# Kernel tuning notes

Hardware: AMD Instinct MI355X
Metric: run time of the kernel (lower is better)

## Reference

```python
import jax, jax.numpy as jnp
import numpy as np

# Config derived from init_kwargs
DIM = 256
DSTATE = 64
DCONV = 3
HEADDIM = 64
CHUNK = 256
NGROUPS = 1
DINNER = int(2.0 * DIM)                 # 512
NHEADS = DINNER // HEADDIM              # 8
CONVDIM = DINNER + 2 * NGROUPS * DSTATE  # 640 (x, B, C share the depthwise conv)
DPROJ = 2 * DINNER + 2 * NGROUPS * DSTATE + NHEADS  # z + xBC + dt


def setup_inputs() -> dict:
    key = jax.random.key(0)
    ks = jax.random.split(key, 8)
    B, H, W = 8, 64, 64
    return dict(
        x=jax.random.normal(ks[0], (B, DIM, H, W), jnp.float32),
        ln_w=jnp.ones((DIM,), jnp.float32),
        ln_b=jnp.zeros((DIM,), jnp.float32),
        in_proj_w=jax.random.normal(ks[1], (DPROJ, DIM), jnp.float32) * 0.02,
        conv_w=jax.random.normal(ks[2], (CONVDIM, 1, DCONV, DCONV), jnp.float32) * 0.1,
        conv_b=jnp.zeros((CONVDIM,), jnp.float32),
        A_log=jnp.log(jax.random.uniform(ks[3], (NHEADS,), jnp.float32, 1.0, 16.0)),
        D=jnp.ones((NHEADS,), jnp.float32),
        dt_bias=jax.random.uniform(ks[4], (NHEADS,), jnp.float32, -2.0, 0.0),
        rms_w=jnp.ones((DINNER,), jnp.float32),
        out_proj_w=jax.random.normal(ks[5], (DIM, DINNER), jnp.float32) * 0.02,
    )


def _ssd(X, dA, Bm, Cm, chunk):
    """Mamba2 SSD chunked parallel scan.
    X:  (b, l, h, p)  inputs already multiplied by dt
    dA: (b, l, h)     dt * A (negative)
    Bm, Cm: (b, l, h, n)
    """
    b, l, h, p = X.shape
    n = Bm.shape[-1]
    c = l // chunk
    q = chunk
    Xc = X.reshape(b, c, q, h, p)
    Bc = Bm.reshape(b, c, q, h, n)
    Cc = Cm.reshape(b, c, q, h, n)
    Ac = dA.reshape(b, c, q, h).transpose(0, 3, 1, 2)            # (b,h,c,q)
    Acs = jnp.cumsum(Ac, axis=-1)                                # (b,h,c,q)
    # intra-chunk (diagonal blocks): causal decay matrix L
    tri = jnp.tril(jnp.ones((q, q), bool))
    Ldec = jnp.where(tri, jnp.exp(Acs[..., :, None] - Acs[..., None, :]), 0.0)
    Y_diag = jnp.einsum('bcqhn,bcshn,bhcqs,bcshp->bcqhp', Cc, Bc, Ldec, Xc)
    # per-chunk final states
    decay_states = jnp.exp(Acs[..., -1:] - Acs)                  # (b,h,c,q)
    states = jnp.einsum('bcqhn,bhcq,bcqhp->bchpn', Bc, decay_states, Xc)
    # inter-chunk recurrence (segment-sum over chunk totals)
    A_last = jnp.pad(Acs[..., -1], ((0, 0), (0, 0), (1, 0)))     # (b,h,c+1)
    ccs = jnp.cumsum(A_last, axis=-1)
    tric = jnp.tril(jnp.ones((c + 1, c + 1), bool))
    decay_chunk = jnp.where(tric, jnp.exp(ccs[..., :, None] - ccs[..., None, :]), 0.0)
    states0 = jnp.concatenate([jnp.zeros_like(states[:, :1]), states], axis=1)
    prev = jnp.einsum('bhzc,bchpn->bzhpn', decay_chunk, states0)[:, :-1]
    # contribution of carried-in state (off-diagonal blocks)
    Y_off = jnp.einsum('bcqhn,bchpn,bhcq->bcqhp', Cc, prev, jnp.exp(Acs))
    return (Y_diag + Y_off).reshape(b, l, h, p)


def _forward(x, ln_w, ln_b, in_proj_w, conv_w, conv_b, A_log, D, dt_bias, rms_w, out_proj_w):
    Bn, Cd, Hh, Ww = x.shape
    L = Hh * Ww
    # LayerNorm over channel dim (channel-first LayerNorm2d)
    mu = jnp.mean(x, axis=1, keepdims=True)
    var = jnp.mean((x - mu) ** 2, axis=1, keepdims=True)
    xn = (x - mu) * jax.lax.rsqrt(var + 1e-5)
    xn = xn * ln_w[None, :, None, None] + ln_b[None, :, None, None]
    # input projection (1x1): -> z | xBC | dt
    zxbcdt = jnp.einsum('bchw,dc->bdhw', xn, in_proj_w)
    z = zxbcdt[:, :DINNER]
    xBC = zxbcdt[:, DINNER:DINNER + CONVDIM]
    dt = zxbcdt[:, DINNER + CONVDIM:]                            # (b, nheads, H, W)
    # depthwise 2D conv + SiLU on xBC
    xBC = jax.lax.conv_general_dilated(
        xBC, conv_w, (1, 1), 'SAME',
        dimension_numbers=('NCHW', 'OIHW', 'NCHW'), feature_group_count=CONVDIM)
    xBC = jax.nn.silu(xBC + conv_b[None, :, None, None])
    # flatten spatial -> sequence, channel-last
    def to_seq(t):
        return t.reshape(Bn, t.shape[1], L).transpose(0, 2, 1)
    xBC, dt, z = to_seq(xBC), to_seq(dt), to_seq(z)
    xs = xBC[..., :DINNER].reshape(Bn, L, NHEADS, HEADDIM)
    Bg = xBC[..., DINNER:DINNER + NGROUPS * DSTATE].reshape(Bn, L, NGROUPS, DSTATE)
    Cg = xBC[..., DINNER + NGROUPS * DSTATE:].reshape(Bn, L, NGROUPS, DSTATE)
    hpg = NHEADS // NGROUPS
    Bm = jnp.repeat(Bg, hpg, axis=2)
    Cm = jnp.repeat(Cg, hpg, axis=2)
    dt = jax.nn.softplus(dt + dt_bias[None, None, :])            # (b, L, nheads)
    A = -jnp.exp(A_log)
    y = _ssd(xs * dt[..., None], dt * A[None, None, :], Bm, Cm, CHUNK)
    y = y + D[None, None, :, None] * xs                          # skip connection
    y = y.reshape(Bn, L, DINNER)
    # gated RMSNorm: norm(y * silu(z)) * w
    y = y * jax.nn.silu(z)
    y = y * jax.lax.rsqrt(jnp.mean(y * y, axis=-1, keepdims=True) + 1e-5) * rms_w
    out = jnp.einsum('bld,cd->blc', y, out_proj_w)
    out = out.transpose(0, 2, 1).reshape(Bn, Cd, Hh, Ww)
    return x + out                                               # residual


def reference(x, ln_w, ln_b, in_proj_w, conv_w, conv_b, A_log, D, dt_bias, rms_w, out_proj_w):
    return _forward(x, ln_w, ln_b, in_proj_w, conv_w, conv_b, A_log, D, dt_bias, rms_w, out_proj_w)
```

## Files before the change

### kernel.cpp

```cpp
#include <hip/hip_runtime.h>
#include <hip/hip_bf16.h>
#include <math.h>

#define DIMC   256
#define LSP    4096
#define BATCH  8
#define DINNER 512
#define NHEADS 8
#define HEADDIM 64
#define DSTATE 64
#define CONVDIM 640
#define DPROJ  1160
#define MPAD   1280
#define CHUNK  256
#define NCHUNK 16

typedef unsigned short u16;
typedef __attribute__((ext_vector_type(8))) unsigned short u16x8;
typedef __attribute__((ext_vector_type(8))) short s16x8;
typedef __attribute__((ext_vector_type(4))) float f32x4;

#define MFMA16(a,b,c) __builtin_amdgcn_mfma_f32_16x16x32_bf16((s16x8)(a),(s16x8)(b),(c),0,0,0)

__device__ __forceinline__ float bf2f(u16 u){ return __uint_as_float(((unsigned int)u)<<16); }
__device__ __forceinline__ u16 f2bf(float f){
  unsigned int x = __float_as_uint(f);
  unsigned int r = (x + 0x7fffu + ((x>>16)&1u)) >> 16;
  return (u16)r;
}
__device__ __forceinline__ float softplusf(float x){ return (x > 20.f) ? x : __logf(1.f + __expf(x)); }
__device__ __forceinline__ float siluf(float x){ return x * __builtin_amdgcn_rcpf(1.f + __expf(-x)); }

__global__ void convert_w(const float* __restrict__ src, u16* __restrict__ dst,
                          int total, int valid){
  int i = blockIdx.x*256 + threadIdx.x;
  if (i >= total) return;
  dst[i] = (i < valid) ? f2bf(src[i]) : (u16)0;
}

__global__ void convert_w_rms(const float* __restrict__ src, const float* __restrict__ rmsw,
                              u16* __restrict__ dst){
  int i = blockIdx.x*256 + threadIdx.x;
  if (i >= DIMC*DINNER) return;
  dst[i] = f2bf(src[i] * rmsw[i & (DINNER-1)]);
}

__global__ void ln_kernel(const float* __restrict__ X, const float* __restrict__ lnw,
                          const float* __restrict__ lnb, u16* __restrict__ XNT) {
  int pos = blockIdx.x*256 + threadIdx.x;
  int b = pos >> 12, l = pos & (LSP-1);
  const float* xb = X + ((size_t)b*DIMC)*LSP + l;
  float sum=0.f, sq=0.f;
  for (int c=0;c<DIMC;c++){ float v=xb[(size_t)c*LSP]; sum+=v; sq+=v*v; }
  float mu = sum*(1.f/DIMC);
  float var = sq*(1.f/DIMC) - mu*mu;
  float rs = rsqrtf(var + 1e-5f);
  u16* ob = XNT + ((size_t)(b*LSP + l))*DIMC;
  for (int c0=0;c0<DIMC;c0+=8){
    u16x8 v8;
    #pragma unroll
    for(int j=0;j<8;j++){
      float v = xb[(size_t)(c0+j)*LSP];
      v8[j] = f2bf((v-mu)*rs*lnw[c0+j] + lnb[c0+j]);
    }
    *(u16x8*)&ob[c0] = v8;
  }
}

__global__ __launch_bounds__(256,2) void gemm_in_fused(
    const u16* __restrict__ W, const u16* __restrict__ XNT,
    u16* __restrict__ ZT, u16* __restrict__ XBC, u16* __restrict__ DT){
  __shared__ u16 Xs[128][264];
  __shared__ u16 Ws[128][32];
  int tid=threadIdx.x, w=tid>>6, lane=tid&63, l15=lane&15, quad=lane>>4;
  int n0=blockIdx.x*128, mh=blockIdx.y, b=blockIdx.z;
  {
    const u16* src = XNT + ((size_t)(b*LSP + n0))*DIMC;
    #pragma unroll
    for (int i=0;i<16;i++){
      int g = i*256 + tid;
      int row = g>>5, c8 = (g&31)*8;
      *(u16x8*)&Xs[row][c8] = *(const u16x8*)&src[(size_t)row*DIMC + c8];
    }
  }
  for (int pti=0; pti<5; pti++){
    int ptg = mh*5 + pti;
    int m0 = ptg*128;
    f32x4 acc[4][4];
    #pragma unroll
    for(int i=0;i<4;i++)
      #pragma unroll
      for(int j=0;j<4;j++) acc[i][j]=(f32x4){0.f,0.f,0.f,0.f};
    for (int k0=0;k0<DIMC;k0+=32){
      __syncthreads();
      {
        int ch = tid*2;
        int r = ch>>2, o=(ch&3)*8;
        *(u16x8*)&Ws[r][o] = *(const u16x8*)&W[(size_t)(m0+r)*DIMC + k0 + o];
        ch++; r = ch>>2; o=(ch&3)*8;
        *(u16x8*)&Ws[r][o] = *(const u16x8*)&W[(size_t)(m0+r)*DIMC + k0 + o];
      }
      __syncthreads();
      u16x8 af[4], bfr[4];
      if (ptg < 4){
        #pragma unroll
        for(int mt=0;mt<4;mt++) af[mt] = *(const u16x8*)&Xs[(w>>1)*64+mt*16+l15][k0+quad*8];
        #pragma unroll
        for(int nt=0;nt<4;nt++) bfr[nt] = *(const u16x8*)&Ws[(w&1)*64+nt*16+l15][quad*8];
      } else {
        #pragma unroll
        for(int mt=0;mt<4;mt++) af[mt] = *(const u16x8*)&Ws[(w>>1)*64+mt*16+l15][quad*8];
        #pragma unroll
        for(int nt=0;nt<4;nt++) bfr[nt] = *(const u16x8*)&Xs[(w&1)*64+nt*16+l15][k0+quad*8];
      }
      #pragma unroll
      for(int mt=0;mt<4;mt++)
        #pragma unroll
        for(int nt=0;nt<4;nt++)
          acc[mt][nt]=MFMA16(af[mt],bfr[nt],acc[mt][nt]);
    }
    if (ptg < 4){
      #pragma unroll
      for(int mt=0;mt<4;mt++)
        #pragma unroll
        for(int nt=0;nt<4;nt++)
          #pragma unroll
          for(int r=0;r<4;r++){
            int lrow = n0 + (w>>1)*64 + mt*16 + quad*4 + r;
            int dcol = m0 + (w&1)*64 + nt*16 + l15;
            ZT[((size_t)b*LSP + lrow)*DINNER + dcol] = f2bf(acc[mt][nt][r]);
          }
    } else {
      #pragma unroll
      for(int mt=0;mt<4;mt++)
        #pragma unroll
        for(int nt=0;nt<4;nt++)
          #pragma unroll
          for(int r=0;r<4;r++){
            int prow = m0 + (w>>1)*64 + mt*16 + quad*4 + r;
            if (prow>=DPROJ) continue;
            int col = n0 + (w&1)*64 + nt*16 + l15;
            u16 v = f2bf(acc[mt][nt][r]);
            if (prow<DINNER+CONVDIM)  XBC[((size_t)b*CONVDIM+(prow-DINNER))*LSP+col]=v;
            else                      DT[((size_t)b*NHEADS+(prow-DINNER-CONVDIM))*LSP+col]=v;
          }
    }
  }
}

__global__ void gemm_out_mfma(const u16* __restrict__ A, const u16* __restrict__ Bm,
                              const float* __restrict__ Res, float* __restrict__ Out){
  __shared__ u16 As[128][32];
  __shared__ u16 Bs[128][32];
  __shared__ float rinv[128];
  int tid=threadIdx.x, w=tid>>6, lane=tid&63, l15=lane&15, quad=lane>>4;
  int b=blockIdx.z, m0=blockIdx.y*128, n0=blockIdx.x*128;
  const u16* Bb = Bm + ((size_t)b*LSP + n0)*DINNER;
  f32x4 acc[4][4];
  #pragma unroll
  for(int i=0;i<4;i++)
    #pragma unroll
    for(int j=0;j<4;j++) acc[i][j] = (f32x4){0.f,0.f,0.f,0.f};
  float sqacc = 0.f;
  for (int k0=0;k0<DINNER;k0+=32){
    __syncthreads();
    {
      int ch = tid*2;
      int r = ch>>2, o=(ch&3)*8;
      *(u16x8*)&As[r][o] = *(const u16x8*)&A[(size_t)(m0+r)*DINNER + k0 + o];
      u16x8 bv = *(const u16x8*)&Bb[(size_t)r*DINNER + k0 + o];
      *(u16x8*)&Bs[r][o] = bv;
      #pragma unroll
      for(int j=0;j<8;j++){ float f=bf2f(bv[j]); sqacc += f*f; }
      ch++; r = ch>>2; o=(ch&3)*8;
      *(u16x8*)&As[r][o] = *(const u16x8*)&A[(size_t)(m0+r)*DINNER + k0 + o];
      u16x8 bv2 = *(const u16x8*)&Bb[(size_t)r*DINNER + k0 + o];
      *(u16x8*)&Bs[r][o] = bv2;
      #pragma unroll
      for(int j=0;j<8;j++){ float f=bf2f(bv2[j]); sqacc += f*f; }
    }
    __syncthreads();
    u16x8 af[4], bfr[4];
    #pragma unroll
    for(int mt=0;mt<4;mt++) af[mt] = *(const u16x8*)&As[(w>>1)*64+mt*16+l15][quad*8];
    #pragma unroll
    for(int nt=0;nt<4;nt++) bfr[nt] = *(const u16x8*)&Bs[(w&1)*64+nt*16+l15][quad*8];
    #pragma unroll
    for(int mt=0;mt<4;mt++)
      #pragma unroll
      for(int nt=0;nt<4;nt++)
        acc[mt][nt]=MFMA16(af[mt],bfr[nt],acc[mt][nt]);
  }
  {
    float tot = sqacc + __shfl_xor(sqacc, 1, 64);
    if ((tid&1)==0) rinv[tid>>1] = rsqrtf(tot*(1.f/DINNER) + 1e-5f);
  }
  __syncthreads();
  #pragma unroll
  for(int mt=0;mt<4;mt++)
    #pragma unroll
    for(int nt=0;nt<4;nt++){
      float rv = rinv[(w&1)*64 + nt*16 + l15];
      #pragma unroll
      for(int r=0;r<4;r++){
        int row = m0 + (w>>1)*64 + mt*16 + quad*4 + r;
        int col = n0 + (w&1)*64 + nt*16 + l15;
        size_t oi = ((size_t)b*DIMC+row)*LSP+col;
        Out[oi] = acc[mt][nt][r]*rv + Res[oi];
      }
    }
}

__global__ void conv_kernel(u16* __restrict__ XBC, const float* __restrict__ CW,
                            const float* __restrict__ CB){
  int ch = blockIdx.x, b = blockIdx.y, tid = threadIdx.x;
  __shared__ float plane[66*66];
  u16* base = XBC + ((size_t)b*CONVDIM + ch)*LSP;
  for (int idx=tid; idx<66*66; idx+=256){
    int yy = idx/66 - 1, xx = idx%66 - 1;
    float v = 0.f;
    if (yy>=0 && yy<64 && xx>=0 && xx<64) v = bf2f(base[yy*64+xx]);
    plane[idx] = v;
  }
  float wg[9];
  #pragma unroll
  for (int t=0;t<9;t++) wg[t] = CW[ch*9+t];
  float bias = CB[ch];
  __syncthreads();
  for (int r=0;r<16;r++){
    int pix = tid + r*256;
    int y = pix>>6, x = pix&63;
    float s=0.f;
    #pragma unroll
    for(int dy=0;dy<3;dy++)
      #pragma unroll
      for(int dx=0;dx<3;dx++) s += plane[(y+dy)*66 + x+dx]*wg[dy*3+dx];
    base[pix] = f2bf(siluf(s + bias));
  }
}

__global__ void ssd_pre_kernel(const u16* __restrict__ DT, const float* __restrict__ A_log,
                               const float* __restrict__ dt_bias, float* __restrict__ ACS,
                               float* __restrict__ DTV, float* __restrict__ DASUM){
  int c=blockIdx.x, h=blockIdx.y, b=blockIdx.z, tid=threadIdx.x;
  __shared__ float acs[CHUNK];
  size_t base = ((size_t)b*NHEADS+h)*LSP + c*CHUNK + tid;
  float raw = bf2f(DT[base]);
  float dtv = softplusf(raw + dt_bias[h]);
  float Ah = -__expf(A_log[h]);
  acs[tid] = dtv*Ah;
  __syncthreads();
  for(int o=1;o<256;o<<=1){
    float add=(tid>=o)?acs[tid-o]:0.f;
    __syncthreads(); acs[tid]+=add; __syncthreads();
  }
  ACS[base] = acs[tid];
  DTV[base] = dtv;
  if (tid==CHUNK-1) DASUM[((size_t)b*NHEADS+h)*NCHUNK+c] = acs[tid];
}

__global__ __launch_bounds__(256,4) void ssd_states_mfma(
    const float* __restrict__ ACS, const float* __restrict__ DTV,
    const float* __restrict__ DASUM, const u16* __restrict__ XBC,
    float* __restrict__ STATES){
  int c=blockIdx.x, h=blockIdx.y, b=blockIdx.z;
  int tid=threadIdx.x, w=tid>>6, lane=tid&63, l15=lane&15, quad=lane>>4;
  __shared__ float wdt[CHUNK];
  __shared__ u16 Xw[64][136];
  __shared__ u16 Bn[64][136];
  {
    size_t base = ((size_t)b*NHEADS+h)*LSP + c*CHUNK + tid;
    float atot = DASUM[((size_t)b*NHEADS+h)*NCHUNK+c];
    wdt[tid] = DTV[base]*__expf(atot - ACS[base]);
  }
  __syncthreads();
  f32x4 acc[4];
  #pragma unroll
  for(int i=0;i<4;i++) acc[i] = (f32x4){0.f,0.f,0.f,0.f};
  size_t cb = (size_t)c*CHUNK;
  for(int th=0; th<2; th++){
    __syncthreads();
    {
      int n=tid&63, q4=tid>>6;
      const u16* Xg = XBC + ((size_t)b*CONVDIM + h*HEADDIM + n)*LSP + cb + th*128;
      const u16* Bg = XBC + ((size_t)b*CONVDIM + DINNER + n)*LSP + cb + th*128;
      #pragma unroll
      for(int i=0;i<4;i++){
        int o = q4*32+i*8;
        u16x8 v = *(const u16x8*)&Xg[o];
        u16x8 wv;
        #pragma unroll
        for(int j=0;j<8;j++) wv[j]=f2bf(bf2f(v[j])*wdt[th*128+o+j]);
        *(u16x8*)&Xw[n][o]=wv;
        *(u16x8*)&Bn[n][o] = *(const u16x8*)&Bg[o];
      }
    }
    __syncthreads();
    #pragma unroll
    for(int k8=0;k8<4;k8++){
      u16x8 a = *(const u16x8*)&Xw[w*16+l15][k8*32+quad*8];
      #pragma unroll
      for(int nt=0;nt<4;nt++){
        u16x8 bb = *(const u16x8*)&Bn[nt*16+l15][k8*32+quad*8];
        acc[nt]=MFMA16(a,bb,acc[nt]);
      }
    }
  }
  float* dst = STATES + (((size_t)b*NHEADS+h)*NCHUNK+c)*4096;
  #pragma unroll
  for(int nt=0;nt<4;nt++)
    #pragma unroll
    for(int r=0;r<4;r++)
      dst[(w*16+quad*4+r)*64 + nt*16+l15] = acc[nt][r];
}

__global__ void ssd_scan_kernel(const float* __restrict__ STATES, const float* __restrict__ DASUM,
                                u16* __restrict__ PREVB){
  int g = blockIdx.x, h = blockIdx.y, b = blockIdx.z, tid = threadIdx.x;
  int e = g*256 + tid;
  size_t hb = (size_t)b*NHEADS + h;
  size_t base = hb*NCHUNK*4096 + e;
  float s = 0.f;
  for (int cc=0;cc<NCHUNK;cc++){
    PREVB[base + (size_t)cc*4096] = f2bf(s);
    s = s*__expf(DASUM[hb*NCHUNK + cc]) + STATES[base + (size_t)cc*4096];
  }
}

__global__ __launch_bounds__(256,3) void ssd_y_mfma(
    const float* __restrict__ ACS, const float* __restrict__ DTV,
    const u16* __restrict__ XBC, const float* __restrict__ Dp,
    const u16* __restrict__ PREVB, const u16* __restrict__ ZT,
    u16* __restrict__ YG){
  int hp = blockIdx.x, bx = blockIdx.y, b = blockIdx.z;
  int h0 = hp*2;
  int c = bx>>2, tb = 3-(bx&3);
  int tid=threadIdx.x, w=tid>>6, lane=tid&63, l15=lane&15, quad=lane>>4;
  __shared__ float acs2[2][CHUNK];
  __shared__ float dtv2[2][CHUNK];
  __shared__ u16 Bs[64][72];
  __shared__ u16 Xs[2][64][72];
  __shared__ u16 Ps[2][64][72];
  {
    size_t base0 = ((size_t)b*NHEADS+h0)*LSP + c*CHUNK + tid;
    acs2[0][tid] = ACS[base0];
    dtv2[0][tid] = DTV[base0];
    acs2[1][tid] = ACS[base0 + LSP];
    dtv2[1][tid] = DTV[base0 + LSP];
  }
  u16x8 ca0, ca1;
  {
    const u16* Cbase = XBC + ((size_t)b*CONVDIM + DINNER + DSTATE)*LSP
                     + (size_t)c*CHUNK + tb*64 + w*16 + l15;
    #pragma unroll
    for(int j=0;j<8;j++){
      ca0[j] = Cbase[(size_t)(quad*8+j)*LSP];
      ca1[j] = Cbase[(size_t)(32+quad*8+j)*LSP];
    }
  }
  __syncthreads();
  f32x4 Yd[2][4], Yo[2][4];
  #pragma unroll
  for(int hh=0;hh<2;hh++)
    #pragma unroll
    for(int i=0;i<4;i++){ Yd[hh][i]=(f32x4){0.f,0.f,0.f,0.f}; Yo[hh][i]=(f32x4){0.f,0.f,0.f,0.f}; }
  #pragma unroll
  for(int hh=0;hh<2;hh++){
    const u16* Pg = PREVB + (((size_t)b*NHEADS+h0+hh)*NCHUNK + c)*4096;
    #pragma unroll
    for(int pt=0;pt<4;pt++){
      u16x8 b0 = *(const u16x8*)&Pg[(pt*16+l15)*64 + quad*8];
      u16x8 b1 = *(const u16x8*)&Pg[(pt*16+l15)*64 + 32 + quad*8];
      Yo[hh][pt]=MFMA16(ca0,b0,Yo[hh][pt]);
      Yo[hh][pt]=MFMA16(ca1,b1,Yo[hh][pt]);
    }
  }
  int tloc = tb*64 + w*16 + quad*4;
  float acst[2][4];
  #pragma unroll
  for(int hh=0;hh<2;hh++)
    #pragma unroll
    for(int r=0;r<4;r++) acst[hh][r] = acs2[hh][tloc+r];
  float DhA[2] = { Dp[h0], Dp[h0+1] };
  for(int sb=0; sb<=tb; sb++){
    __syncthreads();
    {
      int n=tid&63, q4=tid>>6;
      const u16* Bg = XBC + ((size_t)b*CONVDIM + DINNER + n)*LSP + (size_t)c*CHUNK + sb*64;
      #pragma unroll
      for(int i=0;i<2;i++){
        u16x8 v = *(const u16x8*)&Bg[q4*16+i*8];
        #pragma unroll
        for(int j=0;j<8;j++) Bs[q4*16+i*8+j][n]=v[j];
      }
      #pragma unroll
      for(int hh=0;hh<2;hh++){
        const u16* Xg = XBC + ((size_t)b*CONVDIM + (h0+hh)*HEADDIM + n)*LSP + (size_t)c*CHUNK + sb*64;
        #pragma unroll
        for(int i=0;i<2;i++){
          int o = q4*16+i*8;
          *(u16x8*)&Xs[hh][n][o] = *(const u16x8*)&Xg[o];
        }
      }
    }
    __syncthreads();
    f32x4 S[4];
    #pragma unroll
    for(int st=0;st<4;st++){
      S[st]=(f32x4){0.f,0.f,0.f,0.f};
      u16x8 b0 = *(const u16x8*)&Bs[st*16+l15][quad*8];
      u16x8 b1 = *(const u16x8*)&Bs[st*16+l15][32+quad*8];
      S[st]=MFMA16(ca0,b0,S[st]);
      S[st]=MFMA16(ca1,b1,S[st]);
    }
    #pragma unroll
    for(int hh=0;hh<2;hh++){
      float Dh = DhA[hh];
      if (sb < tb){
        #pragma unroll
        for(int st=0;st<4;st++){
          int s = sb*64 + st*16 + l15;
          float as = acs2[hh][s], dv = dtv2[hh][s];
          #pragma unroll
          for(int r=0;r<4;r++)
            Ps[hh][w*16+quad*4+r][st*16+l15] = f2bf(S[st][r]*__expf(acst[hh][r]-as)*dv);
        }
      } else {
        #pragma unroll
        for(int st=0;st<4;st++){
          int s = sb*64 + st*16 + l15;
          float as = acs2[hh][s], dv = dtv2[hh][s];
          #pragma unroll
          for(int r=0;r<4;r++){
            int t = tloc + r;
            float pv;
            if (s < t)       pv = S[st][r]*__expf(acst[hh][r]-as)*dv;
            else if (s == t) pv = S[st][r]*dv + Dh;
            else             pv = 0.f;
            Ps[hh][w*16+quad*4+r][st*16+l15] = f2bf(pv);
          }
        }
      }
      u16x8 p0 = *(const u16x8*)&Ps[hh][w*16+l15][quad*8];
      u16x8 p1 = *(const u16x8*)&Ps[hh][w*16+l15][32+quad*8];
      #pragma unroll
      for(int pt=0;pt<4;pt++){
        u16x8 x0 = *(const u16x8*)&Xs[hh][pt*16+l15][quad*8];
        u16x8 x1 = *(const u16x8*)&Xs[hh][pt*16+l15][32+quad*8];
        Yd[hh][pt]=MFMA16(p0,x0,Yd[hh][pt]);
        Yd[hh][pt]=MFMA16(p1,x1,Yd[hh][pt]);
      }
    }
  }
  __syncthreads();
  typedef float f32row[66];
  f32row* Yf0 = (f32row*)Ps;
  f32row* Yf1 = (f32row*)Xs;
  {
    float eat0[4], eat1[4];
    #pragma unroll
    for(int r=0;r<4;r++){ eat0[r]=__expf(acst[0][r]); eat1[r]=__expf(acst[1][r]); }
    #pragma unroll
    for(int pt=0;pt<4;pt++)
      #pragma unroll
      for(int r=0;r<4;r++){
        int row = w*16 + quad*4 + r;
        Yf0[row][pt*16+l15] = Yd[0][pt][r] + eat0[r]*Yo[0][pt][r];
        Yf1[row][pt*16+l15] = Yd[1][pt][r] + eat1[r]*Yo[1][pt][r];
      }
  }
  __syncthreads();
  {
    int row = tid>>2, seg = tid&3;
    size_t lrow = (size_t)b*LSP + (size_t)c*CHUNK + tb*64 + row;
    #pragma unroll
    for(int hh=0;hh<2;hh++){
      f32row* Yf = hh ? Yf1 : Yf0;
      size_t oi = lrow*DINNER + (size_t)(h0+hh)*HEADDIM + seg*16;
      u16x8 z0 = *(const u16x8*)&ZT[oi];
      u16x8 z1 = *(const u16x8*)&ZT[oi+8];
      u16x8 o0, o1;
      #pragma unroll
      for(int j=0;j<8;j++){
        o0[j] = f2bf(Yf[row][seg*16+j]   * siluf(bf2f(z0[j])));
        o1[j] = f2bf(Yf[row][seg*16+8+j] * siluf(bf2f(z1[j])));
      }
      *(u16x8*)&YG[oi]   = o0;
      *(u16x8*)&YG[oi+8] = o1;
    }
  }
}

extern "C" void kernel_launch(void* const* d_in, const int* in_sizes, int n_in,
                              void* d_out, int out_size, void* d_ws, size_t ws_size,
                              hipStream_t stream) {
  const float* x     = (const float*)d_in[0];
  const float* lnw   = (const float*)d_in[1];
  const float* lnb   = (const float*)d_in[2];
  const float* inpw  = (const float*)d_in[3];
  const float* convw = (const float*)d_in[4];
  const float* convb = (const float*)d_in[5];
  const float* alog  = (const float*)d_in[6];
  const float* Dp    = (const float*)d_in[7];
  const float* dtbi  = (const float*)d_in[8];
  const float* rmsw  = (const float*)d_in[9];
  const float* outw  = (const float*)d_in[10];
  float* out = (float*)d_out;

  char* ws = (char*)d_ws;
  size_t off = 0;
  auto alloc = [&](size_t bytes)->void*{ void* p = ws+off; off += (bytes+255)&~(size_t)255; return p; };
  u16*   WPIN   = (u16*)  alloc((size_t)MPAD*DIMC*2);
  u16*   WPOUT  = (u16*)  alloc((size_t)DIMC*DINNER*2);
  char*  RA     = (char*) alloc((size_t)BATCH*NHEADS*NCHUNK*4096*4);
  u16*   XNT    = (u16*)RA;
  float* STATES = (float*)RA;
  u16*   ZT     = (u16*)  alloc((size_t)BATCH*LSP*DINNER*2);
  u16*   XBC    = (u16*)  alloc((size_t)BATCH*CONVDIM*LSP*2);
  u16*   DTb    = (u16*)  alloc((size_t)BATCH*NHEADS*LSP*2);
  u16*   PREVB  = (u16*)  alloc((size_t)BATCH*NHEADS*NCHUNK*4096*2);
  float* DASUM  = (float*)alloc((size_t)BATCH*NHEADS*NCHUNK*4);
  float* ACS    = (float*)alloc((size_t)BATCH*NHEADS*LSP*4);
  float* DTV    = (float*)alloc((size_t)BATCH*NHEADS*LSP*4);
  u16*   YG     = (u16*)  alloc((size_t)BATCH*LSP*DINNER*2);

  convert_w<<<(MPAD*DIMC+255)/256,256,0,stream>>>(inpw, WPIN, MPAD*DIMC, DPROJ*DIMC);
  convert_w_rms<<<(DIMC*DINNER+255)/256,256,0,stream>>>(outw, rmsw, WPOUT);
  ln_kernel<<<dim3(BATCH*LSP/256),256,0,stream>>>(x,lnw,lnb,XNT);
  gemm_in_fused<<<dim3(LSP/128,2,BATCH),256,0,stream>>>(WPIN, XNT, ZT, XBC, DTb);
  conv_kernel<<<dim3(CONVDIM,BATCH),256,0,stream>>>(XBC, convw, convb);
  ssd_pre_kernel<<<dim3(NCHUNK,NHEADS,BATCH),256,0,stream>>>(DTb, alog, dtbi, ACS, DTV, DASUM);
  ssd_states_mfma<<<dim3(NCHUNK,NHEADS,BATCH),256,0,stream>>>(ACS,DTV,DASUM,XBC,STATES);
  ssd_scan_kernel<<<dim3(16,NHEADS,BATCH),256,0,stream>>>(STATES,DASUM,PREVB);
  ssd_y_mfma<<<dim3(NHEADS/2,NCHUNK*4,BATCH),256,0,stream>>>(ACS,DTV,XBC,Dp,PREVB,ZT,YG);
  gemm_out_mfma<<<dim3(LSP/128,DIMC/128,BATCH),256,0,stream>>>(WPOUT, YG, x, out);
}
```

Measured before the change: 318.8 us.

## Slim ssd_y shared memory, double-buffer B tile, read X directly, use exp2

```diff
diff --git a/kernel.cpp b/kernel.cpp
--- a/kernel.cpp
+++ b/kernel.cpp
@@ -14,6 +14,7 @@
 #define MPAD   1280
 #define CHUNK  256
 #define NCHUNK 16
+#define LOG2E  1.44269504088896f
 
 typedef unsigned short u16;
 typedef __attribute__((ext_vector_type(8))) unsigned short u16x8;
@@ -28,6 +29,7 @@
   unsigned int r = (x + 0x7fffu + ((x>>16)&1u)) >> 16;
   return (u16)r;
 }
+__device__ __forceinline__ float exp2g(float x){ return __builtin_amdgcn_exp2f(x); }
 __device__ __forceinline__ float softplusf(float x){ return (x > 20.f) ? x : __logf(1.f + __expf(x)); }
 __device__ __forceinline__ float siluf(float x){ return x * __builtin_amdgcn_rcpf(1.f + __expf(-x)); }
 
@@ -248,7 +250,7 @@
   float raw = bf2f(DT[base]);
   float dtv = softplusf(raw + dt_bias[h]);
   float Ah = -__expf(A_log[h]);
-  acs[tid] = dtv*Ah;
+  acs[tid] = dtv*Ah*LOG2E;
   __syncthreads();
   for(int o=1;o<256;o<<=1){
     float add=(tid>=o)?acs[tid-o]:0.f;
@@ -271,7 +273,7 @@
   {
     size_t base = ((size_t)b*NHEADS+h)*LSP + c*CHUNK + tid;
     float atot = DASUM[((size_t)b*NHEADS+h)*NCHUNK+c];
-    wdt[tid] = DTV[base]*__expf(atot - ACS[base]);
+    wdt[tid] = DTV[base]*exp2g(atot - ACS[base]);
   }
   __syncthreads();
   f32x4 acc[4];
@@ -323,11 +325,11 @@
   float s = 0.f;
   for (int cc=0;cc<NCHUNK;cc++){
     PREVB[base + (size_t)cc*4096] = f2bf(s);
-    s = s*__expf(DASUM[hb*NCHUNK + cc]) + STATES[base + (size_t)cc*4096];
-  }
-}
-
-__global__ __launch_bounds__(256,3) void ssd_y_mfma(
+    s = s*exp2g(DASUM[hb*NCHUNK + cc]) + STATES[base + (size_t)cc*4096];
+  }
+}
+
+__global__ __launch_bounds__(256,5) void ssd_y_mfma(
     const float* __restrict__ ACS, const float* __restrict__ DTV,
     const u16* __restrict__ XBC, const float* __restrict__ Dp,
     const u16* __restrict__ PREVB, const u16* __restrict__ ZT,
@@ -336,17 +338,19 @@
   int h0 = hp*2;
   int c = bx>>2, tb = 3-(bx&3);
   int tid=threadIdx.x, w=tid>>6, lane=tid&63, l15=lane&15, quad=lane>>4;
-  __shared__ float acs2[2][CHUNK];
-  __shared__ float dtv2[2][CHUNK];
-  __shared__ u16 Bs[64][72];
-  __shared__ u16 Xs[2][64][72];
-  __shared__ u16 Ps[2][64][72];
+  __shared__ __align__(16) char smem[31744];
+  float* acs2 = (float*)smem;
+  float* dtv2 = (float*)(smem+2048);
+  typedef u16 u16row72[72];
+  u16row72* BsA = (u16row72*)(smem+4096);
+  u16row72* BsB = (u16row72*)(smem+4096+9216);
+  u16row72* Ps  = (u16row72*)(smem+22528);
   {
     size_t base0 = ((size_t)b*NHEADS+h0)*LSP + c*CHUNK + tid;
-    acs2[0][tid] = ACS[base0];
-    dtv2[0][tid] = DTV[base0];
-    acs2[1][tid] = ACS[base0 + LSP];
-    dtv2[1][tid] = DTV[base0 + LSP];
+    acs2[tid]     = ACS[base0];
+    dtv2[tid]     = DTV[base0];
+    acs2[256+tid] = ACS[base0+LSP];
+    dtv2[256+tid] = DTV[base0+LSP];
   }
   u16x8 ca0, ca1;
   {
@@ -359,48 +363,42 @@
     }
   }
   __syncthreads();
-  f32x4 Yd[2][4], Yo[2][4];
+  int tloc = tb*64 + w*16 + quad*4;
+  float acst[2][4], eat2[2][4];
   #pragma unroll
   for(int hh=0;hh<2;hh++)
     #pragma unroll
-    for(int i=0;i<4;i++){ Yd[hh][i]=(f32x4){0.f,0.f,0.f,0.f}; Yo[hh][i]=(f32x4){0.f,0.f,0.f,0.f}; }
+    for(int r=0;r<4;r++){
+      acst[hh][r] = acs2[hh*256 + tloc + r];
+      eat2[hh][r] = exp2g(acst[hh][r]);
+    }
+  float DhA[2] = { Dp[h0], Dp[h0+1] };
+  f32x4 Yd[2][4];
   #pragma unroll
   for(int hh=0;hh<2;hh++){
     const u16* Pg = PREVB + (((size_t)b*NHEADS+h0+hh)*NCHUNK + c)*4096;
     #pragma unroll
     for(int pt=0;pt<4;pt++){
+      f32x4 yo = (f32x4){0.f,0.f,0.f,0.f};
       u16x8 b0 = *(const u16x8*)&Pg[(pt*16+l15)*64 + quad*8];
       u16x8 b1 = *(const u16x8*)&Pg[(pt*16+l15)*64 + 32 + quad*8];
-      Yo[hh][pt]=MFMA16(ca0,b0,Yo[hh][pt]);
-      Yo[hh][pt]=MFMA16(ca1,b1,Yo[hh][pt]);
-    }
-  }
-  int tloc = tb*64 + w*16 + quad*4;
-  float acst[2][4];
-  #pragma unroll
-  for(int hh=0;hh<2;hh++)
-    #pragma unroll
-    for(int r=0;r<4;r++) acst[hh][r] = acs2[hh][tloc+r];
-  float DhA[2] = { Dp[h0], Dp[h0+1] };
+      yo = MFMA16(ca0,b0,yo);
+      yo = MFMA16(ca1,b1,yo);
+      #pragma unroll
+      for(int r=0;r<4;r++) Yd[hh][pt][r] = eat2[hh][r]*yo[r];
+    }
+  }
+  const u16* Bgbase = XBC + ((size_t)b*CONVDIM + DINNER)*LSP + (size_t)c*CHUNK;
   for(int sb=0; sb<=tb; sb++){
-    __syncthreads();
+    u16row72* Bsb = (sb&1) ? BsB : BsA;
     {
       int n=tid&63, q4=tid>>6;
-      const u16* Bg = XBC + ((size_t)b*CONVDIM + DINNER + n)*LSP + (size_t)c*CHUNK + sb*64;
+      const u16* Bg = Bgbase + (size_t)n*LSP + sb*64;
       #pragma unroll
       for(int i=0;i<2;i++){
         u16x8 v = *(const u16x8*)&Bg[q4*16+i*8];
         #pragma unroll
-        for(int j=0;j<8;j++) Bs[q4*16+i*8+j][n]=v[j];
-      }
-      #pragma unroll
-      for(int hh=0;hh<2;hh++){
-        const u16* Xg = XBC + ((size_t)b*CONVDIM + (h0+hh)*HEADDIM + n)*LSP + (size_t)c*CHUNK + sb*64;
-        #pragma unroll
-        for(int i=0;i<2;i++){
-          int o = q4*16+i*8;
-          *(u16x8*)&Xs[hh][n][o] = *(const u16x8*)&Xg[o];
-        }
+        for(int j=0;j<8;j++) Bsb[q4*16+i*8+j][n]=v[j];
       }
     }
     __syncthreads();
@@ -408,74 +406,69 @@
     #pragma unroll
     for(int st=0;st<4;st++){
       S[st]=(f32x4){0.f,0.f,0.f,0.f};
-      u16x8 b0 = *(const u16x8*)&Bs[st*16+l15][quad*8];
-      u16x8 b1 = *(const u16x8*)&Bs[st*16+l15][32+quad*8];
+      u16x8 b0 = *(const u16x8*)&Bsb[st*16+l15][quad*8];
+      u16x8 b1 = *(const u16x8*)&Bsb[st*16+l15][32+quad*8];
       S[st]=MFMA16(ca0,b0,S[st]);
       S[st]=MFMA16(ca1,b1,S[st]);
     }
     #pragma unroll
     for(int hh=0;hh<2;hh++){
       float Dh = DhA[hh];
+      const float* acsh = acs2 + hh*256;
+      const float* dtvh = dtv2 + hh*256;
       if (sb < tb){
         #pragma unroll
         for(int st=0;st<4;st++){
           int s = sb*64 + st*16 + l15;
-          float as = acs2[hh][s], dv = dtv2[hh][s];
+          float as = acsh[s], dv = dtvh[s];
           #pragma unroll
           for(int r=0;r<4;r++)
-            Ps[hh][w*16+quad*4+r][st*16+l15] = f2bf(S[st][r]*__expf(acst[hh][r]-as)*dv);
+            Ps[w*16+quad*4+r][st*16+l15] = f2bf(S[st][r]*exp2g(acst[hh][r]-as)*dv);
         }
       } else {
         #pragma unroll
         for(int st=0;st<4;st++){
           int s = sb*64 + st*16 + l15;
-          float as = acs2[hh][s], dv = dtv2[hh][s];
+          float as = acsh[s], dv = dtvh[s];
           #pragma unroll
           for(int r=0;r<4;r++){
             int t = tloc + r;
             float pv;
-            if (s < t)       pv = S[st][r]*__expf(acst[hh][r]-as)*dv;
+            if (s < t)       pv = S[st][r]*exp2g(acst[hh][r]-as)*dv;
             else if (s == t) pv = S[st][r]*dv + Dh;
             else             pv = 0.f;
-            Ps[hh][w*16+quad*4+r][st*16+l15] = f2bf(pv);
+            Ps[w*16+quad*4+r][st*16+l15] = f2bf(pv);
           }
         }
       }
-      u16x8 p0 = *(const u16x8*)&Ps[hh][w*16+l15][quad*8];
-      u16x8 p1 = *(const u16x8*)&Ps[hh][w*16+l15][32+quad*8];
+      u16x8 p0 = *(const u16x8*)&Ps[w*16+l15][quad*8];
+      u16x8 p1 = *(const u16x8*)&Ps[w*16+l15][32+quad*8];
+      const u16* Xg = XBC + ((size_t)b*CONVDIM + (h0+hh)*HEADDIM)*LSP
+                    + (size_t)c*CHUNK + sb*64;
       #pragma unroll
       for(int pt=0;pt<4;pt++){
-        u16x8 x0 = *(const u16x8*)&Xs[hh][pt*16+l15][quad*8];
-        u16x8 x1 = *(const u16x8*)&Xs[hh][pt*16+l15][32+quad*8];
+        const u16* xr = Xg + (size_t)(pt*16+l15)*LSP + quad*8;
+        u16x8 x0 = *(const u16x8*)&xr[0];
+        u16x8 x1 = *(const u16x8*)&xr[32];
         Yd[hh][pt]=MFMA16(p0,x0,Yd[hh][pt]);
         Yd[hh][pt]=MFMA16(p1,x1,Yd[hh][pt]);
       }
     }
   }
   __syncthreads();
-  typedef float f32row[66];
-  f32row* Yf0 = (f32row*)Ps;
-  f32row* Yf1 = (f32row*)Xs;
-  {
-    float eat0[4], eat1[4];
-    #pragma unroll
-    for(int r=0;r<4;r++){ eat0[r]=__expf(acst[0][r]); eat1[r]=__expf(acst[1][r]); }
+  typedef float f32row66[66];
+  f32row66* Yf = (f32row66*)smem;
+  #pragma unroll
+  for(int hh=0;hh<2;hh++){
     #pragma unroll
     for(int pt=0;pt<4;pt++)
       #pragma unroll
-      for(int r=0;r<4;r++){
-        int row = w*16 + quad*4 + r;
-        Yf0[row][pt*16+l15] = Yd[0][pt][r] + eat0[r]*Yo[0][pt][r];
-        Yf1[row][pt*16+l15] = Yd[1][pt][r] + eat1[r]*Yo[1][pt][r];
-      }
-  }
-  __syncthreads();
-  {
-    int row = tid>>2, seg = tid&3;
-    size_t lrow = (size_t)b*LSP + (size_t)c*CHUNK + tb*64 + row;
-    #pragma unroll
-    for(int hh=0;hh<2;hh++){
-      f32row* Yf = hh ? Yf1 : Yf0;
+      for(int r=0;r<4;r++)
+        Yf[w*16+quad*4+r][pt*16+l15] = Yd[hh][pt][r];
+    __syncthreads();
+    {
+      int row = tid>>2, seg = tid&3;
+      size_t lrow = (size_t)b*LSP + (size_t)c*CHUNK + tb*64 + row;
       size_t oi = lrow*DINNER + (size_t)(h0+hh)*HEADDIM + seg*16;
       u16x8 z0 = *(const u16x8*)&ZT[oi];
       u16x8 z1 = *(const u16x8*)&ZT[oi+8];
@@ -488,6 +481,7 @@
       *(u16x8*)&YG[oi]   = o0;
       *(u16x8*)&YG[oi+8] = o1;
     }
+    if (hh==0) __syncthreads();
   }
 }
 
```

Measured after the change: 384.4 us. +20.6%, slower.
